# Kernel optimization log

Measured on AMD Instinct MI355X. Metric: run time of the kernel, lower is better.

The kernel has to match this reference:

```python
import jax, jax.numpy as jnp
import numpy as np

N = 100000      # nodes
E = 1600000     # directed edges (before self loops)
F_IN = 128      # n_features
H = 100         # hidden width of every GCNConv / fc1
N_HIDDEN = 8    # conv2..conv9


def setup_inputs() -> dict:
    key = jax.random.key(0)
    ks = jax.random.split(key, 12)
    s = 0.05
    x = jax.random.normal(ks[0], (N, F_IN), jnp.float32)
    edge_index = jax.random.randint(ks[1], (2, E), 0, N, dtype=jnp.int64)
    labels = (jax.random.uniform(ks[2], (N, 1)) < 0.1).astype(jnp.float32)
    W1 = jax.random.normal(ks[3], (F_IN, H), jnp.float32) * s
    b1 = jnp.zeros((H,), jnp.float32)
    Wh = jax.random.normal(ks[4], (N_HIDDEN, H, H), jnp.float32) * s
    bh = jnp.zeros((N_HIDDEN, H), jnp.float32)
    fc1_W = jax.random.normal(ks[5], (H, H), jnp.float32) * s
    fc1_b = jnp.zeros((H,), jnp.float32)
    fc2_W = jax.random.normal(ks[6], (H, 1), jnp.float32) * s
    fc2_b = jnp.zeros((1,), jnp.float32)
    return {"x": x, "edge_index": edge_index, "labels": labels,
            "W1": W1, "b1": b1, "Wh": Wh, "bh": bh,
            "fc1_W": fc1_W, "fc1_b": fc1_b, "fc2_W": fc2_W, "fc2_b": fc2_b}


def _gcn_conv(h, W, b, src, dst, norm):
    # linear transform, then degree-normalized scatter aggregation (PyG GCNConv)
    h = h @ W                                   # [N, H]
    msg = h[src] * norm[:, None]                # [E2, H] gather + scale
    agg = jax.ops.segment_sum(msg, dst, num_segments=N)  # scatter-add to [N, H]
    return agg + b


def reference(x, edge_index, labels, W1, b1, Wh, bh, fc1_W, fc1_b, fc2_W, fc2_b):
    # GCN normalization with self loops: norm_e = deg^-1/2[src] * deg^-1/2[dst]
    loops = jnp.arange(N, dtype=edge_index.dtype)
    src = jnp.concatenate([edge_index[0], loops])
    dst = jnp.concatenate([edge_index[1], loops])
    deg = jax.ops.segment_sum(jnp.ones_like(dst, jnp.float32), dst, num_segments=N)
    dinv = jax.lax.rsqrt(deg)                   # deg >= 1 due to self loops
    norm = dinv[src] * dinv[dst]

    # NOTE: source uses x.relu() (out-of-place, discarded) -> no nonlinearity;
    # dropout is identity in eval mode. Faithful reproduction below.
    h = _gcn_conv(x, W1, b1, src, dst, norm)
    for i in range(N_HIDDEN):
        h = _gcn_conv(h, Wh[i], bh[i], src, dst, norm)

    h = h @ fc1_W + fc1_b
    logits = h @ fc2_W + fc2_b
    p = jax.nn.sigmoid(logits)                  # [N, 1]

    # generate_weights: upweight positives by neg/pos ratio
    pos = labels.sum()
    w = ((jnp.float32(N) - pos) / pos) * labels + 1.0

    pc = jnp.clip(p, 1e-7, 1.0 - 1e-7)
    bce = -(labels * jnp.log(pc) + (1.0 - labels) * jnp.log(1.0 - pc))
    loss = jnp.mean(w * bce)
    return loss, p
```

## Files before the change

kernel.cpp:

```cpp
#include <hip/hip_runtime.h>
#include <math.h>

#define HW 100
#define FIN 128
#define NBLK 256
#define TPB 1024
#define CHUNK 392
#define PBLK 512
#define BCAP 64
#define ELDS 7424
#define M17 0x1FFFFu

typedef int iv4 __attribute__((ext_vector_type(4)));
typedef unsigned long long ull;

__device__ __forceinline__ float ld_dev(const float* p) {
    return __hip_atomic_load(p, __ATOMIC_RELAXED, __HIP_MEMORY_SCOPE_AGENT);
}
__device__ __forceinline__ unsigned ld_devu(const unsigned* p) {
    return __hip_atomic_load(p, __ATOMIC_RELAXED, __HIP_MEMORY_SCOPE_AGENT);
}
__device__ __forceinline__ ull ld_u64(const ull* p) {
    return __hip_atomic_load(p, __ATOMIC_RELAXED, __HIP_MEMORY_SCOPE_AGENT);
}
__device__ __forceinline__ void st_u64(ull* p, ull v) {
    __hip_atomic_store(p, v, __ATOMIC_RELAXED, __HIP_MEMORY_SCOPE_AGENT);
}

__device__ __forceinline__ float gwait(const ull* p, unsigned want) {
    ull v = ld_u64(p);
    while ((unsigned)(v >> 32) != want) { __builtin_amdgcn_s_sleep(1); v = ld_u64(p); }
    return __uint_as_float((unsigned)v);
}

__global__ void k_initchain(float* __restrict__ accums, unsigned* __restrict__ posDone,
                            unsigned* __restrict__ fin, unsigned* __restrict__ epoch,
                            const float* __restrict__ W1, const float* __restrict__ b1,
                            const float* __restrict__ Wh, const float* __restrict__ bh,
                            const float* __restrict__ fc1W, const float* __restrict__ fc1b,
                            const float* __restrict__ fc2W, const float* __restrict__ fc2b,
                            float* __restrict__ wstar, float* __restrict__ gammas) {
    __shared__ float v[HW], vn[HW];
    int t = threadIdx.x;
    if (t < HW) v[t] = fc2W[t];
    __syncthreads();
    if (t < HW) { float a = 0.f; for (int c = 0; c < HW; ++c) a += fc1W[t * HW + c] * v[c]; vn[t] = a; }
    __syncthreads();
    if (t < HW) v[t] = vn[t];
    __syncthreads();
    if (t == 0) {
        float a = 0.f; for (int c = 0; c < HW; ++c) a += bh[7 * HW + c] * v[c];
        float b = 0.f; for (int c = 0; c < HW; ++c) b += fc1b[c] * fc2W[c];
        gammas[9] = a + b + fc2b[0];
    }
    __syncthreads();
    for (int i = 7; i >= 0; --i) {
        const float* M = Wh + (size_t)i * HW * HW;
        if (t < HW) { float a = 0.f; for (int c = 0; c < HW; ++c) a += M[t * HW + c] * v[c]; vn[t] = a; }
        __syncthreads();
        if (t < HW) v[t] = vn[t];
        __syncthreads();
        if (t == 0) {
            const float* bb = (i >= 1) ? (bh + (size_t)(i - 1) * HW) : b1;
            float a = 0.f; for (int c = 0; c < HW; ++c) a += bb[c] * v[c];
            gammas[i + 1] = a;
        }
        __syncthreads();
    }
    if (t < FIN) { float a = 0.f; for (int c = 0; c < HW; ++c) a += W1[t * HW + c] * v[c]; wstar[t] = a; }
    if (t == 0) {
        accums[0] = 0.f; accums[1] = 0.f;
        *posDone = 0u; *fin = 0u;
        *epoch = *epoch + 1u;
    }
}

__global__ __launch_bounds__(256) void k_part(const int* __restrict__ src,
                                              const int* __restrict__ dst, int E4,
                                              unsigned* __restrict__ buckets,
                                              int* __restrict__ cnt) {
    __shared__ int cur[NBLK];
    int tid = threadIdx.x;
    if (tid < NBLK) cur[tid] = 0;
    __syncthreads();
    const iv4* d4 = reinterpret_cast<const iv4*>(dst);
    const iv4* s4 = reinterpret_cast<const iv4*>(src);
    int i = blockIdx.x * 256 + tid;
    int stride = gridDim.x * 256;
    for (; i < E4; i += stride) {
        iv4 d = __builtin_nontemporal_load(d4 + i);
        iv4 s = __builtin_nontemporal_load(s4 + i);
        #pragma unroll
        for (int q = 0; q < 4; ++q) {
            unsigned dd = (unsigned)d[q];
            unsigned ss = (unsigned)s[q];
            unsigned c = (unsigned)(((ull)dd * 171634ull) >> 26);
            unsigned ldst = dd - c * 391u;
            int pos = atomicAdd(&cur[c], 1);
            if (pos < BCAP)
                buckets[((size_t)c * PBLK + blockIdx.x) * BCAP + pos] = ss | (ldst << 17);
        }
    }
    __syncthreads();
    if (tid < NBLK) cnt[(size_t)blockIdx.x * NBLK + tid] = cur[tid];
}

__global__ __launch_bounds__(TPB) void k_main(const float* __restrict__ x,
        const float* __restrict__ labels,
        const float* __restrict__ wstar, const float* __restrict__ gammas,
        const int* __restrict__ cntG, const unsigned* __restrict__ bucketsG,
        ull* __restrict__ u0buf, ull* __restrict__ u1buf, ull* __restrict__ u2buf,
        float* __restrict__ accums, unsigned* __restrict__ posDone,
        unsigned* __restrict__ fin, const unsigned* __restrict__ epoch,
        float* __restrict__ outF, int N) {
    __shared__ alignas(16) float ws[FIN];
    __shared__ float gam[16];
    __shared__ int   cntL[PBLK], incl[PBLK];
    __shared__ int   degLi[CHUNK];
    __shared__ float dinvL[CHUNK], uownL[CHUNK], yownL[CHUNK], accL[CHUNK];
    __shared__ float red[TPB];
    __shared__ unsigned myE[ELDS];

    int tid = threadIdx.x;
    int b = blockIdx.x;
    int chunk = (N + NBLK - 1) / NBLK;
    int nlo = b * chunk; if (nlo > N) nlo = N;
    int nhi = nlo + chunk; if (nhi > N) nhi = N;
    int nn = nhi - nlo;
    unsigned tagb = (*epoch) * 16u;

    if (tid < FIN) ws[tid] = wstar[tid];
    if (tid < 16) gam[tid] = gammas[tid];
    for (int r = tid; r < CHUNK; r += TPB) degLi[r] = 0;
    if (tid < PBLK) { int v = cntG[(size_t)tid * NBLK + b]; cntL[tid] = v; incl[tid] = v; }
    __syncthreads();
    for (int off = 1; off < PBLK; off <<= 1) {
        int v = (tid < PBLK && tid >= off) ? incl[tid - off] : 0;
        __syncthreads();
        if (tid < PBLK) incl[tid] += v;
        __syncthreads();
    }
    int ecnt = incl[PBLK - 1];
    if (ecnt > ELDS) ecnt = ELDS;

    const unsigned* col = bucketsG + (size_t)b * PBLK * BCAP;
    for (int idx = tid; idx < PBLK * BCAP; idx += TPB) {
        int p = idx >> 6, j = idx & (BCAP - 1);
        int c = cntL[p];
        if (j < c) {
            unsigned e = col[(size_t)p * BCAP + j];
            int o = incl[p] - c + j;
            if (o < ELDS) { myE[o] = e; atomicAdd(&degLi[e >> 17], 1); }
        }
    }
    __syncthreads();
    for (int r = tid; r < nn; r += TPB) dinvL[r] = rsqrtf((float)degLi[r] + 1.0f);
    __syncthreads();

    {
        int wid = tid >> 6, half = (tid >> 5) & 1, l32 = tid & 31;
        int pcnt = (nn + 1) >> 1;
        const float4* x4 = reinterpret_cast<const float4*>(x);
        for (int pb = wid; pb < pcnt; pb += 16) {
            int ln = pb * 2 + half;
            float dsum = 0.f;
            if (ln < nn) {
                float4 xv = x4[(size_t)(nlo + ln) * (FIN / 4) + l32];
                float4 wv = *reinterpret_cast<const float4*>(&ws[l32 * 4]);
                dsum = xv.x * wv.x + xv.y * wv.y + xv.z * wv.z + xv.w * wv.w;
            }
            #pragma unroll
            for (int off = 16; off; off >>= 1) dsum += __shfl_down(dsum, off, 32);
            if (l32 == 0 && ln < nn) {
                float u0 = dsum * dinvL[ln];
                uownL[ln] = u0;
                st_u64(&u0buf[nlo + ln], (ull)__float_as_uint(u0) | ((ull)tagb << 32));
            }
        }
    }
    {
        float s = 0.f;
        for (int ln = tid; ln < nn; ln += TPB) s += labels[nlo + ln];
        red[tid] = s; __syncthreads();
        for (int off = TPB / 2; off; off >>= 1) {
            if (tid < off) red[tid] += red[tid + off];
            __syncthreads();
        }
        if (tid == 0) {
            atomicAdd(&accums[0], red[0]);
            asm volatile("s_waitcnt vmcnt(0)" ::: "memory");
            __hip_atomic_fetch_add(posDone, 1u, __ATOMIC_RELAXED, __HIP_MEMORY_SCOPE_AGENT);
        }
    }

    ull* bufs[3] = {u0buf, u1buf, u2buf};
    for (int k = 1; k <= 9; ++k) {
        unsigned want = tagb + (unsigned)(k - 1);
        const ull* ubr = bufs[(k - 1) % 3];
        ull* ubw = bufs[k % 3];
        float gk = gam[k];
        for (int ln = tid; ln < nn; ln += TPB) accL[ln] = uownL[ln];
        __syncthreads();
        int e = tid;
        for (; e + 3 * TPB < ecnt; e += 4 * TPB) {
            unsigned p0 = myE[e], p1 = myE[e + TPB], p2 = myE[e + 2 * TPB], p3 = myE[e + 3 * TPB];
            const ull* a0 = &ubr[p0 & M17];
            const ull* a1 = &ubr[p1 & M17];
            const ull* a2 = &ubr[p2 & M17];
            const ull* a3 = &ubr[p3 & M17];
            ull v0 = ld_u64(a0), v1 = ld_u64(a1), v2 = ld_u64(a2), v3 = ld_u64(a3);
            float f0 = ((unsigned)(v0 >> 32) == want) ? __uint_as_float((unsigned)v0) : gwait(a0, want);
            float f1 = ((unsigned)(v1 >> 32) == want) ? __uint_as_float((unsigned)v1) : gwait(a1, want);
            float f2 = ((unsigned)(v2 >> 32) == want) ? __uint_as_float((unsigned)v2) : gwait(a2, want);
            float f3 = ((unsigned)(v3 >> 32) == want) ? __uint_as_float((unsigned)v3) : gwait(a3, want);
            atomicAdd(&accL[p0 >> 17], f0);
            atomicAdd(&accL[p1 >> 17], f1);
            atomicAdd(&accL[p2 >> 17], f2);
            atomicAdd(&accL[p3 >> 17], f3);
        }
        for (; e < ecnt; e += TPB) {
            unsigned p = myE[e];
            float f = gwait(&ubr[p & M17], want);
            atomicAdd(&accL[p >> 17], f);
        }
        __syncthreads();
        for (int ln = tid; ln < nn; ln += TPB) {
            float di = dinvL[ln];
            float y = di * accL[ln] + gk;
            float nu = di * y;
            uownL[ln] = nu;
            if (k < 9) st_u64(&ubw[nlo + ln], (ull)__float_as_uint(nu) | ((ull)(tagb + k) << 32));
            else yownL[ln] = y;
        }
        __syncthreads();
    }

    if (tid == 0)
        while (ld_devu(posDone) < NBLK) __builtin_amdgcn_s_sleep(2);
    __syncthreads();
    {
        float pos = ld_dev(&accums[0]);
        float wpos = ((float)N - pos) / pos;
        float acc = 0.f;
        for (int ln = tid; ln < nn; ln += TPB) {
            float y = yownL[ln];
            float pp = 1.f / (1.f + expf(-y));
            outF[1 + nlo + ln] = pp;
            float pc = fminf(fmaxf(pp, 1e-7f), 1.f - 1e-7f);
            float l = labels[nlo + ln];
            float w = wpos * l + 1.f;
            acc += w * (-(l * logf(pc) + (1.f - l) * logf(1.f - pc)));
        }
        red[tid] = acc; __syncthreads();
        for (int off = TPB / 2; off; off >>= 1) {
            if (tid < off) red[tid] += red[tid + off];
            __syncthreads();
        }
        if (tid == 0) {
            atomicAdd(&accums[1], red[0]);
            asm volatile("s_waitcnt vmcnt(0)" ::: "memory");
            unsigned old = __hip_atomic_fetch_add(fin, 1u, __ATOMIC_RELAXED, __HIP_MEMORY_SCOPE_AGENT);
            if (old == NBLK - 1u)
                outF[0] = ld_dev(&accums[1]) / (float)N;
        }
    }
}

extern "C" void kernel_launch(void* const* d_in, const int* in_sizes, int n_in,
                              void* d_out, int out_size, void* d_ws, size_t ws_size,
                              hipStream_t stream) {
    const float* x      = (const float*)d_in[0];
    const int*   edge   = (const int*)d_in[1];
    const float* labels = (const float*)d_in[2];
    const float* W1     = (const float*)d_in[3];
    const float* b1     = (const float*)d_in[4];
    const float* Wh     = (const float*)d_in[5];
    const float* bh     = (const float*)d_in[6];
    const float* fc1W   = (const float*)d_in[7];
    const float* fc1b   = (const float*)d_in[8];
    const float* fc2W   = (const float*)d_in[9];
    const float* fc2b   = (const float*)d_in[10];

    const int N = in_sizes[0] / FIN;
    const int E = in_sizes[1] / 2;
    const int* srcIdx = edge;
    const int* dstIdx = edge + E;

    size_t o = 0;
    auto carve = [&](size_t bytes) {
        void* p = (char*)d_ws + o;
        o += (bytes + 511) & ~(size_t)511;
        return p;
    };
    float*    accums  = (float*)   carve(4 * 4);
    unsigned* posDone = (unsigned*)carve(4);
    unsigned* fin     = (unsigned*)carve(4);
    unsigned* epoch   = (unsigned*)carve(4);
    float*    wstar   = (float*)   carve(FIN * 4);
    float*    gammas  = (float*)   carve(16 * 4);
    ull*      u0buf   = (ull*)     carve((size_t)N * 8);
    ull*      u1buf   = (ull*)     carve((size_t)N * 8);
    ull*      u2buf   = (ull*)     carve((size_t)N * 8);
    int*      cnt     = (int*)     carve((size_t)PBLK * NBLK * 4);
    unsigned* buckets = (unsigned*)carve((size_t)NBLK * PBLK * BCAP * 4);
    (void)ws_size; (void)n_in; (void)out_size;

    k_initchain<<<1, 256, 0, stream>>>(accums, posDone, fin, epoch,
                                       W1, b1, Wh, bh, fc1W, fc1b, fc2W, fc2b,
                                       wstar, gammas);
    k_part<<<PBLK, 256, 0, stream>>>(srcIdx, dstIdx, E / 4, buckets, cnt);

    float* outF = (float*)d_out;
    int Nv = N;
    void* args[] = {(void*)&x, (void*)&labels, (void*)&wstar, (void*)&gammas,
                    (void*)&cnt, (void*)&buckets,
                    (void*)&u0buf, (void*)&u1buf, (void*)&u2buf,
                    (void*)&accums, (void*)&posDone, (void*)&fin, (void*)&epoch,
                    (void*)&outF, (void*)&Nv};
    hipError_t err = hipLaunchCooperativeKernel((const void*)k_main, dim3(NBLK), dim3(TPB),
                                                args, 0, stream);
    (void)err;
}
```

Before: 191.5 us.

## Replace per-element epoch-tagged values with per-block flags and float double buffers

Per-element 64-bit tagged values with per-element spin checks are replaced by plain 32-bit float double buffers. Each block now publishes a progress flag after each layer and waits until every block has reached that layer before gathering. This halves the bytes fetched in the random gather and drops the per-load tag comparisons. Edge indices are also read from LDS as uint4. The cost is a coarser, barrier-like wait on all blocks in place of fine-grained dataflow, plus a flag reset in the init kernel.

New measurement: 458.2 us. 2.39x slower.

```diff
diff --git a/kernel.cpp b/kernel.cpp
--- a/kernel.cpp
+++ b/kernel.cpp
@@ -12,29 +12,22 @@
 #define M17 0x1FFFFu
 
 typedef int iv4 __attribute__((ext_vector_type(4)));
-typedef unsigned long long ull;
 
 __device__ __forceinline__ float ld_dev(const float* p) {
     return __hip_atomic_load(p, __ATOMIC_RELAXED, __HIP_MEMORY_SCOPE_AGENT);
 }
+__device__ __forceinline__ void st_dev(float* p, float v) {
+    __hip_atomic_store(p, v, __ATOMIC_RELAXED, __HIP_MEMORY_SCOPE_AGENT);
+}
 __device__ __forceinline__ unsigned ld_devu(const unsigned* p) {
     return __hip_atomic_load(p, __ATOMIC_RELAXED, __HIP_MEMORY_SCOPE_AGENT);
 }
-__device__ __forceinline__ ull ld_u64(const ull* p) {
-    return __hip_atomic_load(p, __ATOMIC_RELAXED, __HIP_MEMORY_SCOPE_AGENT);
-}
-__device__ __forceinline__ void st_u64(ull* p, ull v) {
+__device__ __forceinline__ void st_devu(unsigned* p, unsigned v) {
     __hip_atomic_store(p, v, __ATOMIC_RELAXED, __HIP_MEMORY_SCOPE_AGENT);
 }
 
-__device__ __forceinline__ float gwait(const ull* p, unsigned want) {
-    ull v = ld_u64(p);
-    while ((unsigned)(v >> 32) != want) { __builtin_amdgcn_s_sleep(1); v = ld_u64(p); }
-    return __uint_as_float((unsigned)v);
-}
-
 __global__ void k_initchain(float* __restrict__ accums, unsigned* __restrict__ posDone,
-                            unsigned* __restrict__ fin, unsigned* __restrict__ epoch,
+                            unsigned* __restrict__ fin, unsigned* __restrict__ flags,
                             const float* __restrict__ W1, const float* __restrict__ b1,
                             const float* __restrict__ Wh, const float* __restrict__ bh,
                             const float* __restrict__ fc1W, const float* __restrict__ fc1b,
@@ -42,6 +35,7 @@
                             float* __restrict__ wstar, float* __restrict__ gammas) {
     __shared__ float v[HW], vn[HW];
     int t = threadIdx.x;
+    for (int i = t; i < NBLK * 16; i += 256) flags[i] = 0u;
     if (t < HW) v[t] = fc2W[t];
     __syncthreads();
     if (t < HW) { float a = 0.f; for (int c = 0; c < HW; ++c) a += fc1W[t * HW + c] * v[c]; vn[t] = a; }
@@ -68,11 +62,7 @@
         __syncthreads();
     }
     if (t < FIN) { float a = 0.f; for (int c = 0; c < HW; ++c) a += W1[t * HW + c] * v[c]; wstar[t] = a; }
-    if (t == 0) {
-        accums[0] = 0.f; accums[1] = 0.f;
-        *posDone = 0u; *fin = 0u;
-        *epoch = *epoch + 1u;
-    }
+    if (t == 0) { accums[0] = 0.f; accums[1] = 0.f; *posDone = 0u; *fin = 0u; }
 }
 
 __global__ __launch_bounds__(256) void k_part(const int* __restrict__ src,
@@ -94,7 +84,7 @@
         for (int q = 0; q < 4; ++q) {
             unsigned dd = (unsigned)d[q];
             unsigned ss = (unsigned)s[q];
-            unsigned c = (unsigned)(((ull)dd * 171634ull) >> 26);
+            unsigned c = (unsigned)(((unsigned long long)dd * 171634ull) >> 26);
             unsigned ldst = dd - c * 391u;
             int pos = atomicAdd(&cur[c], 1);
             if (pos < BCAP)
@@ -109,9 +99,9 @@
         const float* __restrict__ labels,
         const float* __restrict__ wstar, const float* __restrict__ gammas,
         const int* __restrict__ cntG, const unsigned* __restrict__ bucketsG,
-        ull* __restrict__ u0buf, ull* __restrict__ u1buf, ull* __restrict__ u2buf,
-        float* __restrict__ accums, unsigned* __restrict__ posDone,
-        unsigned* __restrict__ fin, const unsigned* __restrict__ epoch,
+        float* __restrict__ ua, float* __restrict__ ub,
+        float* __restrict__ accums, unsigned* __restrict__ flags,
+        unsigned* __restrict__ posDone, unsigned* __restrict__ fin,
         float* __restrict__ outF, int N) {
     __shared__ alignas(16) float ws[FIN];
     __shared__ float gam[16];
@@ -119,7 +109,7 @@
     __shared__ int   degLi[CHUNK];
     __shared__ float dinvL[CHUNK], uownL[CHUNK], yownL[CHUNK], accL[CHUNK];
     __shared__ float red[TPB];
-    __shared__ unsigned myE[ELDS];
+    __shared__ alignas(16) unsigned myE[ELDS];
 
     int tid = threadIdx.x;
     int b = blockIdx.x;
@@ -127,7 +117,6 @@
     int nlo = b * chunk; if (nlo > N) nlo = N;
     int nhi = nlo + chunk; if (nhi > N) nhi = N;
     int nn = nhi - nlo;
-    unsigned tagb = (*epoch) * 16u;
 
     if (tid < FIN) ws[tid] = wstar[tid];
     if (tid < 16) gam[tid] = gammas[tid];
@@ -174,10 +163,11 @@
             if (l32 == 0 && ln < nn) {
                 float u0 = dsum * dinvL[ln];
                 uownL[ln] = u0;
-                st_u64(&u0buf[nlo + ln], (ull)__float_as_uint(u0) | ((ull)tagb << 32));
+                st_dev(&ua[nlo + ln], u0);
             }
         }
     }
+    asm volatile("s_waitcnt vmcnt(0)" ::: "memory");
     {
         float s = 0.f;
         for (int ln = tid; ln < nn; ln += TPB) s += labels[nlo + ln];
@@ -190,38 +180,34 @@
             atomicAdd(&accums[0], red[0]);
             asm volatile("s_waitcnt vmcnt(0)" ::: "memory");
             __hip_atomic_fetch_add(posDone, 1u, __ATOMIC_RELAXED, __HIP_MEMORY_SCOPE_AGENT);
-        }
-    }
-
-    ull* bufs[3] = {u0buf, u1buf, u2buf};
+            st_devu(&flags[b * 16], 1u);
+        }
+    }
+
     for (int k = 1; k <= 9; ++k) {
-        unsigned want = tagb + (unsigned)(k - 1);
-        const ull* ubr = bufs[(k - 1) % 3];
-        ull* ubw = bufs[k % 3];
+        const float* ubr = ((k - 1) & 1) ? ub : ua;
+        float* ubw = (k & 1) ? ub : ua;
         float gk = gam[k];
         for (int ln = tid; ln < nn; ln += TPB) accL[ln] = uownL[ln];
-        __syncthreads();
-        int e = tid;
-        for (; e + 3 * TPB < ecnt; e += 4 * TPB) {
-            unsigned p0 = myE[e], p1 = myE[e + TPB], p2 = myE[e + 2 * TPB], p3 = myE[e + 3 * TPB];
-            const ull* a0 = &ubr[p0 & M17];
-            const ull* a1 = &ubr[p1 & M17];
-            const ull* a2 = &ubr[p2 & M17];
-            const ull* a3 = &ubr[p3 & M17];
-            ull v0 = ld_u64(a0), v1 = ld_u64(a1), v2 = ld_u64(a2), v3 = ld_u64(a3);
-            float f0 = ((unsigned)(v0 >> 32) == want) ? __uint_as_float((unsigned)v0) : gwait(a0, want);
-            float f1 = ((unsigned)(v1 >> 32) == want) ? __uint_as_float((unsigned)v1) : gwait(a1, want);
-            float f2 = ((unsigned)(v2 >> 32) == want) ? __uint_as_float((unsigned)v2) : gwait(a2, want);
-            float f3 = ((unsigned)(v3 >> 32) == want) ? __uint_as_float((unsigned)v3) : gwait(a3, want);
-            atomicAdd(&accL[p0 >> 17], f0);
-            atomicAdd(&accL[p1 >> 17], f1);
-            atomicAdd(&accL[p2 >> 17], f2);
-            atomicAdd(&accL[p3 >> 17], f3);
-        }
-        for (; e < ecnt; e += TPB) {
+        if (tid < NBLK)
+            while (ld_devu(&flags[tid * 16]) < (unsigned)k) __builtin_amdgcn_s_sleep(1);
+        __syncthreads();
+        __builtin_amdgcn_fence(__ATOMIC_ACQUIRE, "agent");
+        int ecnt4 = ecnt & ~3;
+        for (int e = tid * 4; e < ecnt4; e += TPB * 4) {
+            uint4 p = *reinterpret_cast<const uint4*>(&myE[e]);
+            float f0 = ubr[p.x & M17];
+            float f1 = ubr[p.y & M17];
+            float f2 = ubr[p.z & M17];
+            float f3 = ubr[p.w & M17];
+            atomicAdd(&accL[p.x >> 17], f0);
+            atomicAdd(&accL[p.y >> 17], f1);
+            atomicAdd(&accL[p.z >> 17], f2);
+            atomicAdd(&accL[p.w >> 17], f3);
+        }
+        for (int e = ecnt4 + tid; e < ecnt; e += TPB) {
             unsigned p = myE[e];
-            float f = gwait(&ubr[p & M17], want);
-            atomicAdd(&accL[p >> 17], f);
+            atomicAdd(&accL[p >> 17], ubr[p & M17]);
         }
         __syncthreads();
         for (int ln = tid; ln < nn; ln += TPB) {
@@ -229,11 +215,16 @@
             float y = di * accL[ln] + gk;
             float nu = di * y;
             uownL[ln] = nu;
-            if (k < 9) st_u64(&ubw[nlo + ln], (ull)__float_as_uint(nu) | ((ull)(tagb + k) << 32));
+            if (k < 9) st_dev(&ubw[nlo + ln], nu);
             else yownL[ln] = y;
         }
-        __syncthreads();
-    }
+        if (k < 9) {
+            asm volatile("s_waitcnt vmcnt(0)" ::: "memory");
+            __syncthreads();
+            if (tid == 0) st_devu(&flags[b * 16], (unsigned)(k + 1));
+        }
+    }
+    __syncthreads();
 
     if (tid == 0)
         while (ld_devu(posDone) < NBLK) __builtin_amdgcn_s_sleep(2);
@@ -295,17 +286,16 @@
     float*    accums  = (float*)   carve(4 * 4);
     unsigned* posDone = (unsigned*)carve(4);
     unsigned* fin     = (unsigned*)carve(4);
-    unsigned* epoch   = (unsigned*)carve(4);
+    unsigned* flags   = (unsigned*)carve((size_t)NBLK * 16 * 4);
     float*    wstar   = (float*)   carve(FIN * 4);
     float*    gammas  = (float*)   carve(16 * 4);
-    ull*      u0buf   = (ull*)     carve((size_t)N * 8);
-    ull*      u1buf   = (ull*)     carve((size_t)N * 8);
-    ull*      u2buf   = (ull*)     carve((size_t)N * 8);
+    float*    ua      = (float*)   carve((size_t)N * 4);
+    float*    ub      = (float*)   carve((size_t)N * 4);
     int*      cnt     = (int*)     carve((size_t)PBLK * NBLK * 4);
     unsigned* buckets = (unsigned*)carve((size_t)NBLK * PBLK * BCAP * 4);
     (void)ws_size; (void)n_in; (void)out_size;
 
-    k_initchain<<<1, 256, 0, stream>>>(accums, posDone, fin, epoch,
+    k_initchain<<<1, 256, 0, stream>>>(accums, posDone, fin, flags,
                                        W1, b1, Wh, bh, fc1W, fc1b, fc2W, fc2b,
                                        wstar, gammas);
     k_part<<<PBLK, 256, 0, stream>>>(srcIdx, dstIdx, E / 4, buckets, cnt);
@@ -314,8 +304,8 @@
     int Nv = N;
     void* args[] = {(void*)&x, (void*)&labels, (void*)&wstar, (void*)&gammas,
                     (void*)&cnt, (void*)&buckets,
-                    (void*)&u0buf, (void*)&u1buf, (void*)&u2buf,
-                    (void*)&accums, (void*)&posDone, (void*)&fin, (void*)&epoch,
+                    (void*)&ua, (void*)&ub,
+                    (void*)&accums, (void*)&flags, (void*)&posDone, (void*)&fin,
                     (void*)&outF, (void*)&Nv};
     hipError_t err = hipLaunchCooperativeKernel((const void*)k_main, dim3(NBLK), dim3(TPB),
                                                 args, 0, stream);
```
